# Performance work log

Measured on AMD Instinct MI355X. Metric: run time of the kernel, lower is better.

Reference implementation:

```python
import jax, jax.numpy as jnp
import numpy as np

N_NODES = 100000
N_EDGES = 1600000
F_IN = 128
UNITS = 128


def setup_inputs() -> dict:
    key = jax.random.key(0)
    k1, k2, k3, k4, k5 = jax.random.split(key, 5)
    X = jax.random.normal(k1, (N_NODES, F_IN), dtype=jnp.float32)
    edge_row = jnp.sort(jax.random.randint(k2, (N_EDGES,), 0, N_NODES, dtype=jnp.int64))
    edge_col = jax.random.randint(k3, (N_EDGES,), 0, N_NODES, dtype=jnp.int64)
    edge_val = jax.random.uniform(k4, (N_EDGES,), dtype=jnp.float32)
    weight = jax.random.normal(k5, (F_IN, UNITS), dtype=jnp.float32) * (1.0 / np.sqrt(F_IN))
    bias = jnp.zeros((UNITS,), dtype=jnp.float32)
    return {"X": X, "edge_row": edge_row, "edge_col": edge_col,
            "edge_val": edge_val, "weight": weight, "bias": bias}


def reference(X, edge_row, edge_col, edge_val, weight, bias):
    # h = X @ W  (dense feature transform)
    h = jnp.matmul(X, weight)                      # [N, units]
    # output = An @ h  as sparse SpMM: gather source rows, scale, scatter-add
    msg = edge_val[:, None] * h[edge_col]          # [E, units]
    agg = jax.ops.segment_sum(msg, edge_row, num_segments=N_NODES)  # [N, units]
    # bias add + sigmoid activation
    return jax.nn.sigmoid(agg + bias)
```

## Files before the change

kernel.cpp:

```cpp
#include <hip/hip_runtime.h>
#include <cstddef>

#define F 128
#define LDB 136

typedef __attribute__((ext_vector_type(8))) short bf16x8;
typedef __attribute__((ext_vector_type(4))) float f32x4;

__device__ __forceinline__ unsigned short f2bf(float f) {
  unsigned int u = __float_as_uint(f);
  u += 0x7fffu + ((u >> 16) & 1u);
  return (unsigned short)(u >> 16);
}

__global__ __launch_bounds__(256) void build_row_ptr(const int* __restrict__ erow,
                                                     int n_edges, int n_nodes,
                                                     int* __restrict__ row_ptr) {
  const int e = blockIdx.x * 256 + threadIdx.x;
  if (e > n_edges) return;
  int r_lo, r_hi, val;
  if (e == 0) {
    r_lo = 0; r_hi = erow[0]; val = 0;
  } else if (e == n_edges) {
    r_lo = erow[n_edges - 1] + 1; r_hi = n_nodes; val = n_edges;
  } else {
    const int rp = erow[e - 1], rc = erow[e];
    r_lo = rp + 1; r_hi = rc; val = e;
  }
  for (int r = r_lo; r <= r_hi; ++r) row_ptr[r] = val;
}

__global__ __launch_bounds__(256) void convert_w(const float* __restrict__ W,
                                                 unsigned short* __restrict__ Wt) {
  const int idx = blockIdx.x * 256 + threadIdx.x;
  const int k = idx >> 7, n = idx & 127;
  Wt[n * F + k] = f2bf(W[idx]);
}

__global__ __launch_bounds__(256) void gemm_mfma(const float* __restrict__ X,
                                                 const unsigned short* __restrict__ Wt,
                                                 unsigned short* __restrict__ H,
                                                 int n_nodes) {
  __shared__ alignas(16) unsigned short Bs[128 * LDB];
  const int tid = threadIdx.x;

  {
    const uint4* src = (const uint4*)Wt;
    #pragma unroll
    for (int i = 0; i < 8; ++i) {
      const int idx = tid + i * 256;
      const int n = idx >> 4, c8 = idx & 15;
      *(uint4*)&Bs[n * LDB + c8 * 8] = src[idx];
    }
  }
  __syncthreads();

  const int wave = tid >> 6;
  const int lane = tid & 63;
  const int l15 = lane & 15;
  const int quad = lane >> 4;
  const int rbase = blockIdx.x * 128 + wave * 32;

  const float* xr[2];
  #pragma unroll
  for (int rt = 0; rt < 2; ++rt) {
    int r = rbase + rt * 16 + l15;
    if (r > n_nodes - 1) r = n_nodes - 1;
    xr[rt] = X + (size_t)r * F;
  }

  f32x4 acc[2][8] = {};

  #pragma unroll
  for (int ks = 0; ks < 4; ++ks) {
    const int k0 = ks * 32 + quad * 8;
    bf16x8 a[2], b[8];
    #pragma unroll
    for (int rt = 0; rt < 2; ++rt) {
      const float4 x0 = *(const float4*)(xr[rt] + k0);
      const float4 x1 = *(const float4*)(xr[rt] + k0 + 4);
      bf16x8 t;
      t[0] = (short)f2bf(x0.x); t[1] = (short)f2bf(x0.y);
      t[2] = (short)f2bf(x0.z); t[3] = (short)f2bf(x0.w);
      t[4] = (short)f2bf(x1.x); t[5] = (short)f2bf(x1.y);
      t[6] = (short)f2bf(x1.z); t[7] = (short)f2bf(x1.w);
      a[rt] = t;
    }
    #pragma unroll
    for (int ct = 0; ct < 8; ++ct)
      b[ct] = *(const bf16x8*)&Bs[(ct * 16 + l15) * LDB + k0];
    #pragma unroll
    for (int rt = 0; rt < 2; ++rt)
      #pragma unroll
      for (int ct = 0; ct < 8; ++ct)
        acc[rt][ct] = __builtin_amdgcn_mfma_f32_16x16x32_bf16(
            a[rt], b[ct], acc[rt][ct], 0, 0, 0);
  }

  #pragma unroll
  for (int rt = 0; rt < 2; ++rt) {
    #pragma unroll
    for (int r = 0; r < 4; ++r) {
      const int row = rbase + rt * 16 + quad * 4 + r;
      if (row < n_nodes) {
        #pragma unroll
        for (int ct = 0; ct < 8; ++ct)
          H[(size_t)row * F + ct * 16 + l15] = f2bf(acc[rt][ct][r]);
      }
    }
  }
}

__global__ __launch_bounds__(256) void spmm_bias_sigmoid(
    const int* __restrict__ row_ptr, const int* __restrict__ ecol,
    const float* __restrict__ eval, const unsigned int* __restrict__ H2,
    const float* __restrict__ bias, float* __restrict__ out, int n_nodes) {
  const int wave = threadIdx.x >> 6;
  const int lane = threadIdx.x & 63;
  const int node = blockIdx.x * 4 + wave;
  if (node >= n_nodes) return;

  const int lo = row_ptr[node];
  const int hi = row_ptr[node + 1];
  const int deg = hi - lo;

  float acc0 = 0.f, acc1 = 0.f;
  for (int base = 0; base < deg; base += 64) {
    int cv = 0;
    float vv = 0.f;
    if (base + lane < deg) {
      const int e = lo + base + lane;
      cv = ecol[e];
      vv = eval[e];
    }
    int cnt = deg - base;
    if (cnt > 64) cnt = 64;
    #pragma unroll 4
    for (int j = 0; j < cnt; ++j) {
      const int c = __builtin_amdgcn_readlane(cv, j);
      const float v =
          __int_as_float(__builtin_amdgcn_readlane(__float_as_int(vv), j));
      const unsigned int h = H2[(size_t)c * (F / 2) + lane];
      acc0 += v * __uint_as_float(h << 16);
      acc1 += v * __uint_as_float(h & 0xffff0000u);
    }
  }

  const float2 b = *(const float2*)&bias[lane * 2];
  float2 o;
  o.x = 1.f / (1.f + expf(-(acc0 + b.x)));
  o.y = 1.f / (1.f + expf(-(acc1 + b.y)));
  *(float2*)&out[(size_t)node * F + lane * 2] = o;
}

extern "C" void kernel_launch(void* const* d_in, const int* in_sizes, int n_in,
                              void* d_out, int out_size, void* d_ws, size_t ws_size,
                              hipStream_t stream) {
  const float* X    = (const float*)d_in[0];
  const int*   erow = (const int*)  d_in[1];
  const int*   ecol = (const int*)  d_in[2];
  const float* eval = (const float*)d_in[3];
  const float* W    = (const float*)d_in[4];
  const float* bias = (const float*)d_in[5];
  float* out = (float*)d_out;

  const int n_nodes = in_sizes[0] / F;
  const int n_edges = in_sizes[1];

  char* ws = (char*)d_ws;
  unsigned short* H = (unsigned short*)ws;
  size_t off = (size_t)n_nodes * F * sizeof(unsigned short);
  int* row_ptr = (int*)(ws + off);
  off += ((size_t)(n_nodes + 1) * sizeof(int) + 15) & ~(size_t)15;
  unsigned short* Wt = (unsigned short*)(ws + off);

  convert_w<<<F * F / 256, 256, 0, stream>>>(W, Wt);
  build_row_ptr<<<(n_edges + 256) / 256, 256, 0, stream>>>(erow, n_edges,
                                                           n_nodes, row_ptr);
  gemm_mfma<<<(n_nodes + 127) / 128, 256, 0, stream>>>(X, Wt, H, n_nodes);
  spmm_bias_sigmoid<<<(n_nodes + 3) / 4, 256, 0, stream>>>(
      row_ptr, ecol, eval, (const unsigned int*)H, bias, out, n_nodes);
}
```

Before: 231.9 us.

## Process four nodes per wave in SpMM with 16-byte gathers; vectorize GEMM stores

The SpMM kernel now gives each 16-lane group of a wave its own node. Each lane gathers a full 16-byte chunk (8 bf16 features) per neighbor, and edge indices are broadcast with ds_bpermute, replacing one node per wave with 4-byte loads. The GEMM swaps its MFMA operands so each lane holds four consecutive columns and can write them as a single 8-byte packed store instead of scalar 2-byte stores. The SpMM change cuts the number of load instructions and raises memory-level parallelism, but nodes sharing a wave iterate up to the group's maximum degree, which wastes lanes when degrees differ.

```diff
diff --git a/kernel.cpp b/kernel.cpp
--- a/kernel.cpp
+++ b/kernel.cpp
@@ -94,18 +94,21 @@
       #pragma unroll
       for (int ct = 0; ct < 8; ++ct)
         acc[rt][ct] = __builtin_amdgcn_mfma_f32_16x16x32_bf16(
-            a[rt], b[ct], acc[rt][ct], 0, 0, 0);
+            b[ct], a[rt], acc[rt][ct], 0, 0, 0);
   }
 
   #pragma unroll
   for (int rt = 0; rt < 2; ++rt) {
-    #pragma unroll
-    for (int r = 0; r < 4; ++r) {
-      const int row = rbase + rt * 16 + quad * 4 + r;
-      if (row < n_nodes) {
-        #pragma unroll
-        for (int ct = 0; ct < 8; ++ct)
-          H[(size_t)row * F + ct * 16 + l15] = f2bf(acc[rt][ct][r]);
+    const int row = rbase + rt * 16 + l15;
+    if (row < n_nodes) {
+      #pragma unroll
+      for (int ct = 0; ct < 8; ++ct) {
+        const unsigned int d0 = (unsigned int)f2bf(acc[rt][ct][0]) |
+                                ((unsigned int)f2bf(acc[rt][ct][1]) << 16);
+        const unsigned int d1 = (unsigned int)f2bf(acc[rt][ct][2]) |
+                                ((unsigned int)f2bf(acc[rt][ct][3]) << 16);
+        uint2 u; u.x = d0; u.y = d1;
+        *(uint2*)&H[(size_t)row * F + ct * 16 + quad * 4] = u;
       }
     }
   }
@@ -113,44 +116,71 @@
 
 __global__ __launch_bounds__(256) void spmm_bias_sigmoid(
     const int* __restrict__ row_ptr, const int* __restrict__ ecol,
-    const float* __restrict__ eval, const unsigned int* __restrict__ H2,
+    const float* __restrict__ eval, const unsigned short* __restrict__ H,
     const float* __restrict__ bias, float* __restrict__ out, int n_nodes) {
   const int wave = threadIdx.x >> 6;
   const int lane = threadIdx.x & 63;
-  const int node = blockIdx.x * 4 + wave;
-  if (node >= n_nodes) return;
-
-  const int lo = row_ptr[node];
-  const int hi = row_ptr[node + 1];
+  const int g = lane >> 4;
+  const int fl = lane & 15;
+  const int node = blockIdx.x * 16 + wave * 4 + g;
+  const bool valid = (node < n_nodes);
+
+  const int lo = valid ? row_ptr[node] : 0;
+  const int hi = valid ? row_ptr[node + 1] : 0;
   const int deg = hi - lo;
 
-  float acc0 = 0.f, acc1 = 0.f;
-  for (int base = 0; base < deg; base += 64) {
-    int cv = 0;
+  int dmax = deg;
+  dmax = max(dmax, __shfl_xor(dmax, 16, 64));
+  dmax = max(dmax, __shfl_xor(dmax, 32, 64));
+
+  const int bpbase = (lane & 48) * 4;
+  const char* Hb = (const char*)H + fl * 16;
+
+  float acc[8] = {};
+  for (int base = 0; base < dmax; base += 16) {
+    int voff = 0;
     float vv = 0.f;
-    if (base + lane < deg) {
-      const int e = lo + base + lane;
-      cv = ecol[e];
+    if (base + fl < deg) {
+      const int e = lo + base + fl;
+      voff = ecol[e] << 8;
       vv = eval[e];
     }
-    int cnt = deg - base;
-    if (cnt > 64) cnt = 64;
+    int cnt = dmax - base;
+    if (cnt > 16) cnt = 16;
     #pragma unroll 4
     for (int j = 0; j < cnt; ++j) {
-      const int c = __builtin_amdgcn_readlane(cv, j);
-      const float v =
-          __int_as_float(__builtin_amdgcn_readlane(__float_as_int(vv), j));
-      const unsigned int h = H2[(size_t)c * (F / 2) + lane];
-      acc0 += v * __uint_as_float(h << 16);
-      acc1 += v * __uint_as_float(h & 0xffff0000u);
-    }
-  }
-
-  const float2 b = *(const float2*)&bias[lane * 2];
-  float2 o;
-  o.x = 1.f / (1.f + expf(-(acc0 + b.x)));
-  o.y = 1.f / (1.f + expf(-(acc1 + b.y)));
-  *(float2*)&out[(size_t)node * F + lane * 2] = o;
+      const int idx = bpbase + j * 4;
+      const int ro = __builtin_amdgcn_ds_bpermute(idx, voff);
+      const float v = __int_as_float(
+          __builtin_amdgcn_ds_bpermute(idx, __float_as_int(vv)));
+      const uint4 h = *(const uint4*)(Hb + ro);
+      acc[0] += v * __uint_as_float(h.x << 16);
+      acc[1] += v * __uint_as_float(h.x & 0xffff0000u);
+      acc[2] += v * __uint_as_float(h.y << 16);
+      acc[3] += v * __uint_as_float(h.y & 0xffff0000u);
+      acc[4] += v * __uint_as_float(h.z << 16);
+      acc[5] += v * __uint_as_float(h.z & 0xffff0000u);
+      acc[6] += v * __uint_as_float(h.w << 16);
+      acc[7] += v * __uint_as_float(h.w & 0xffff0000u);
+    }
+  }
+
+  if (valid) {
+    const float4 b0 = *(const float4*)&bias[fl * 8];
+    const float4 b1 = *(const float4*)&bias[fl * 8 + 4];
+    float4 o0, o1;
+    o0.x = 1.f / (1.f + expf(-(acc[0] + b0.x)));
+    o0.y = 1.f / (1.f + expf(-(acc[1] + b0.y)));
+    o0.z = 1.f / (1.f + expf(-(acc[2] + b0.z)));
+    o0.w = 1.f / (1.f + expf(-(acc[3] + b0.w)));
+    o1.x = 1.f / (1.f + expf(-(acc[4] + b1.x)));
+    o1.y = 1.f / (1.f + expf(-(acc[5] + b1.y)));
+    o1.z = 1.f / (1.f + expf(-(acc[6] + b1.z)));
+    o1.w = 1.f / (1.f + expf(-(acc[7] + b1.w)));
+    float* op = out + (size_t)node * F + fl * 8;
+    *(float4*)op = o0;
+    *(float4*)(op + 4) = o1;
+  }
 }
 
 extern "C" void kernel_launch(void* const* d_in, const int* in_sizes, int n_in,
@@ -178,6 +208,6 @@
   build_row_ptr<<<(n_edges + 256) / 256, 256, 0, stream>>>(erow, n_edges,
                                                            n_nodes, row_ptr);
   gemm_mfma<<<(n_nodes + 127) / 128, 256, 0, stream>>>(X, Wt, H, n_nodes);
-  spmm_bias_sigmoid<<<(n_nodes + 3) / 4, 256, 0, stream>>>(
-      row_ptr, ecol, eval, (const unsigned int*)H, bias, out, n_nodes);
-}
+  spmm_bias_sigmoid<<<(n_nodes + 15) / 16, 256, 0, stream>>>(
+      row_ptr, ecol, eval, H, bias, out, n_nodes);
+}
```

Measured after the change: 196.7 us. 1.18x faster.
